# Kernel optimization log

Measured on AMD Instinct MI355X. Metric: run time of the kernel, lower is better.

The kernel has to match this reference:

```python
import jax, jax.numpy as jnp
import numpy as np

DEPTH = 16          # levels in the complete binary tree
D_IN = 256
H = 256
K = 2               # n_children
N_NODES = 2 ** DEPTH - 1  # 65535, heap/level order: children of node p at level l are (2p, 2p+1) at level l+1


def setup_inputs() -> dict:
    key = jax.random.key(0)
    ks = jax.random.split(key, 14)
    s = 0.05
    emb = jax.random.normal(ks[0], (N_NODES, D_IN), dtype=jnp.float32)
    mk = lambda k, shape: (jax.random.normal(k, shape, dtype=jnp.float32) * s)
    return {
        "emb": emb,
        "W_i": mk(ks[1], (H, D_IN)), "b_i": mk(ks[2], (H,)), "U_i": mk(ks[3], (K, H, H)),
        "W_o": mk(ks[4], (H, D_IN)), "b_o": mk(ks[5], (H,)), "U_o": mk(ks[6], (K, H, H)),
        "W_u": mk(ks[7], (H, D_IN)), "b_u": mk(ks[8], (H,)), "U_u": mk(ks[9], (K, H, H)),
        "W_f": mk(ks[10], (H, D_IN)), "b_f": mk(ks[11], (H,)), "U_f": mk(ks[12], (K, H, H)),
    }


def _node_batch(x, ch_h, ch_c, W_i, b_i, U_i, W_o, b_o, U_o, W_u, b_u, U_u, W_f, b_f, U_f):
    # x: [n, D_IN]; ch_h, ch_c: [n, K, H]
    # Linear: x @ W.T + b (torch layout W=[out,in]); U_k h = h @ U[k].T
    def gate(W, b, U):
        return x @ W.T + b + jnp.einsum("nkh,kdh->nd", ch_h, U)
    i = jax.nn.sigmoid(gate(W_i, b_i, U_i))
    o = jax.nn.sigmoid(gate(W_o, b_o, U_o))
    u = jnp.tanh(gate(W_u, b_u, U_u))
    # per-child forget gates: f_k = sigmoid(W_f x + U_f[k] h_k)
    f = jax.nn.sigmoid((x @ W_f.T + b_f)[:, None, :] + jnp.einsum("nkh,kdh->nkd", ch_h, U_f))
    c = i * u + jnp.sum(f * ch_c, axis=1)
    h = o * jnp.tanh(c)
    return h, c


def reference(emb, W_i, b_i, U_i, W_o, b_o, U_o, W_u, b_u, U_u, W_f, b_f, U_f):
    params = (W_i, b_i, U_i, W_o, b_o, U_o, W_u, b_u, U_u, W_f, b_f, U_f)
    # leaves: level DEPTH-1, zero children (matches zero-padding in node_forward)
    n = 2 ** (DEPTH - 1)
    start = n - 1
    zeros = jnp.zeros((n, K, H), dtype=emb.dtype)
    h, c = _node_batch(emb[start:start + n], zeros, zeros, *params)
    # bottom-up over internal levels; children of position p are (2p, 2p+1) in level below
    for l in range(DEPTH - 2, -1, -1):
        n = 2 ** l
        start = n - 1
        ch_h = h.reshape(n, K, H)
        ch_c = c.reshape(n, K, H)
        h, c = _node_batch(emb[start:start + n], ch_h, ch_c, *params)
    return h[0], c[0]  # root (hidden, cell), each [H]
```

## Files before the change

kernel.cpp:

```cpp
#include <hip/hip_runtime.h>
#include <hip/hip_bf16.h>
#include <cstdint>
#include <cstddef>


typedef __attribute__((ext_vector_type(8))) __bf16 bf16x8;
typedef __attribute__((ext_vector_type(4))) float floatx4;

#define TB 64

__device__ __forceinline__ float sigf(float x) { return 1.0f / (1.0f + __expf(-x)); }

__device__ __forceinline__ void load_lds16(const void* g, void* l) {
    __builtin_amdgcn_global_load_lds(
        (const __attribute__((address_space(1))) unsigned int*)g,
        (__attribute__((address_space(3))) unsigned int*)l, 16, 0, 0);
}

__global__ void pack_weights(const float* __restrict__ Wi, const float* __restrict__ bi, const float* __restrict__ Ui,
                             const float* __restrict__ Wo, const float* __restrict__ bo, const float* __restrict__ Uo,
                             const float* __restrict__ Wu, const float* __restrict__ bu, const float* __restrict__ Uu,
                             const float* __restrict__ Wf, const float* __restrict__ bf, const float* __restrict__ Uf,
                             __hip_bfloat16* __restrict__ Wpack, float* __restrict__ biasv)
{
    int m = blockIdx.x;
    int d = blockIdx.y;
    int k = threadIdx.x;
    const float* tbl[12] = {Wi, Wo, Wu, Wf,
                            Ui, Uo, Uu, Uf,
                            Ui + 65536, Uo + 65536, Uu + 65536, Uf + 65536};
    Wpack[((size_t)m * 256 + d) * 256 + k] = __float2bfloat16(tbl[m][d * 256 + k]);
    if (m < 4 && k == 0) {
        const float* bt[4] = {bi, bo, bu, bf};
        biasv[m * 256 + d] = bt[m][d];
    }
}

__global__ void convert_f32_bf16(const float* __restrict__ in, __hip_bfloat16* __restrict__ out, int n4)
{
    int i = blockIdx.x * 256 + threadIdx.x;
    if (i >= n4) return;
    float4 v = ((const float4*)in)[i];
    __hip_bfloat16 tmp[4];
    tmp[0] = __float2bfloat16(v.x);
    tmp[1] = __float2bfloat16(v.y);
    tmp[2] = __float2bfloat16(v.z);
    tmp[3] = __float2bfloat16(v.w);
    *(ushort4*)(out + (size_t)i * 4) = *(const ushort4*)tmp;
}

__global__ __launch_bounds__(256) void gemm_zx(
    const __hip_bfloat16* __restrict__ embB,
    const __hip_bfloat16* __restrict__ Wpack,
    const float* __restrict__ biasv,
    float* __restrict__ preZ,
    int M)
{
    __shared__ __hip_bfloat16 sA[64 * 32];
    __shared__ __hip_bfloat16 sB[64 * 32];
    const int t = threadIdx.x;
    const int s = blockIdx.x >> 2;
    const int d0 = (blockIdx.x & 3) * 64;
    const int bm0 = blockIdx.y * 64;
    const int lane = t & 63, w = t >> 6, lrow = lane & 15, q = lane >> 4;

    floatx4 acc[4];
    #pragma unroll
    for (int mt = 0; mt < 4; ++mt) acc[mt] = (floatx4){0.f, 0.f, 0.f, 0.f};

    for (int kk = 0; kk < 8; ++kk) {
        const int k0 = kk * 32;
        {
            int r = t >> 2, kc = t & 3;
            load_lds16(embB + (size_t)(bm0 + r) * 256 + k0 + kc * 8, &sA[t * 8]);
            load_lds16(Wpack + (size_t)(s * 256 + d0 + r) * 256 + k0 + kc * 8, &sB[t * 8]);
        }
        __syncthreads();
        bf16x8 af[4];
        #pragma unroll
        for (int mt = 0; mt < 4; ++mt)
            af[mt] = *(const bf16x8*)&sA[(mt * 16 + lrow) * 32 + q * 8];
        bf16x8 bfr = *(const bf16x8*)&sB[(w * 16 + lrow) * 32 + q * 8];
        #pragma unroll
        for (int mt = 0; mt < 4; ++mt)
            acc[mt] = __builtin_amdgcn_mfma_f32_16x16x32_bf16(af[mt], bfr, acc[mt], 0, 0, 0);
        __syncthreads();
    }

    const int d = d0 + w * 16 + lrow;
    const float bv = biasv[s * 256 + d];
    #pragma unroll
    for (int mt = 0; mt < 4; ++mt)
        #pragma unroll
        for (int rr = 0; rr < 4; ++rr) {
            int m = bm0 + mt * 16 + q * 4 + rr;
            if (m < M) preZ[(size_t)m * 1024 + s * 256 + d] = acc[mt][rr] + bv;
        }
}

template<int NS, int NP>
__global__ __launch_bounds__(256) void fused_level(
    const __hip_bfloat16* __restrict__ embX,
    const __hip_bfloat16* __restrict__ hprev,
    const float* __restrict__ cprev,
    const __hip_bfloat16* __restrict__ Wpack,
    const float* __restrict__ biasv,
    __hip_bfloat16* __restrict__ hout,
    float* __restrict__ cout,
    int M)
{
    __shared__ __hip_bfloat16 sA[64 * 32];
    __shared__ __hip_bfloat16 sB[NS * 64 * 32];
    const int t = threadIdx.x;
    const int dchunk = blockIdx.x;
    const int bm0 = blockIdx.y * 64;
    const int lane = t & 63;
    const int w = t >> 6;
    const int lrow = lane & 15;
    const int q = lane >> 4;

    floatx4 accS[3][4];
    floatx4 accF[NP][4];
    #pragma unroll
    for (int s = 0; s < 3; ++s)
        #pragma unroll
        for (int mt = 0; mt < 4; ++mt) accS[s][mt] = (floatx4){0.f, 0.f, 0.f, 0.f};
    #pragma unroll
    for (int p = 0; p < NP; ++p)
        #pragma unroll
        for (int mt = 0; mt < 4; ++mt) accF[p][mt] = (floatx4){0.f, 0.f, 0.f, 0.f};

    #pragma unroll
    for (int p = 0; p < NP; ++p) {
        const __hip_bfloat16* Abase = (p == 0) ? embX : hprev;
        const int astride = (p == 0) ? 256 : 512;
        const int aoff = (p == 0) ? 0 : (p - 1) * 256;
        for (int kk = 0; kk < 8; ++kk) {
            const int k0 = kk * 32;
            {
                int r = t >> 2, kc = t & 3;
                load_lds16(Abase + (size_t)(bm0 + r) * astride + aoff + k0 + kc * 8,
                           &sA[t * 8]);
            }
            #pragma unroll
            for (int rep = 0; rep < NS; ++rep) {
                int cid = rep * 256 + t;
                int row = cid >> 2, kc = cid & 3;
                int s = row >> 6, r = row & 63;
                load_lds16(Wpack + (size_t)((p * 4 + s) * 256 + dchunk * 64 + r) * 256 + k0 + kc * 8,
                           &sB[cid * 8]);
            }
            __syncthreads();

            bf16x8 af[4];
            #pragma unroll
            for (int mt = 0; mt < 4; ++mt)
                af[mt] = *(const bf16x8*)&sA[(mt * 16 + lrow) * 32 + q * 8];
            #pragma unroll
            for (int s = 0; s < NS; ++s) {
                bf16x8 bfrag = *(const bf16x8*)&sB[(s * 64 + w * 16 + lrow) * 32 + q * 8];
                if (s < 3) {
                    #pragma unroll
                    for (int mt = 0; mt < 4; ++mt)
                        accS[s][mt] = __builtin_amdgcn_mfma_f32_16x16x32_bf16(af[mt], bfrag, accS[s][mt], 0, 0, 0);
                } else {
                    #pragma unroll
                    for (int mt = 0; mt < 4; ++mt)
                        accF[p][mt] = __builtin_amdgcn_mfma_f32_16x16x32_bf16(af[mt], bfrag, accF[p][mt], 0, 0, 0);
                }
            }
            __syncthreads();
        }
    }

    const int d = dchunk * 64 + w * 16 + lrow;
    const float bI = biasv[d];
    const float bO = biasv[256 + d];
    const float bU = biasv[512 + d];
    const float bF = (NS == 4) ? biasv[768 + d] : 0.0f;
    #pragma unroll
    for (int mt = 0; mt < 4; ++mt) {
        #pragma unroll
        for (int rr = 0; rr < 4; ++rr) {
            const int m = bm0 + mt * 16 + q * 4 + rr;
            if (m >= M) continue;
            float iv = sigf(accS[0][mt][rr] + bI);
            float ov = sigf(accS[1][mt][rr] + bO);
            float uv = tanhf(accS[2][mt][rr] + bU);
            float c;
            if (NS == 4) {
                float fx = accF[0][mt][rr];
                float fl = sigf(fx + accF[NP >= 2 ? 1 : 0][mt][rr] + bF);
                float fr = sigf(fx + accF[NP >= 3 ? 2 : 0][mt][rr] + bF);
                c = iv * uv + fl * cprev[(size_t)m * 512 + d]
                            + fr * cprev[(size_t)m * 512 + 256 + d];
            } else {
                c = iv * uv;
            }
            cout[(size_t)m * 256 + d] = c;
            hout[(size_t)m * 256 + d] = __float2bfloat16(ov * tanhf(c));
        }
    }
}

__global__ __launch_bounds__(256) void tail_levels(
    __hip_bfloat16* __restrict__ hbuf, float* __restrict__ cbuf,
    const __hip_bfloat16* __restrict__ Wpack,
    const float* __restrict__ preZ,
    unsigned* __restrict__ bar, float* __restrict__ out)
{
    __shared__ __hip_bfloat16 sB[8 * 16 * 256];
    const int bid = blockIdx.x;
    const int t = threadIdx.x;
    const int dt = bid & 15;
    const int g = bid >> 4;
    const int w = t >> 6, lane = t & 63, lrow = lane & 15, q = lane >> 4;

    for (int rnd = 0; rnd < 16; ++rnd) {
        int C = rnd * 256 + t;
        int q8k = C & 31, r = (C >> 5) & 15, m8 = C >> 9;
        load_lds16(Wpack + (size_t)((4 + m8) * 256 + dt * 16 + r) * 256 + q8k * 8,
                   &sB[(size_t)C * 8]);
    }
    __syncthreads();

    const int d = dt * 16 + lrow;
    unsigned barnum = 0;

    for (int l = 10; l >= 0; --l) {
        const int n = 1 << l;
        const int start = n - 1;
        const int startc = 2 * n - 1;
        const __hip_bfloat16* hp = hbuf + (size_t)startc * 256;
        const float* cp = cbuf + (size_t)startc * 256;
        __hip_bfloat16* ho = hbuf + (size_t)start * 256;
        float* co = cbuf + (size_t)start * 256;
        const int nmt = (n + 15) >> 4;

        for (int mt = g * 4 + w; mt < nmt; mt += 16) {
            const int m0 = mt * 16;
            bf16x8 af[2][8];
            #pragma unroll
            for (int p = 0; p < 2; ++p)
                #pragma unroll
                for (int kk = 0; kk < 8; ++kk)
                    af[p][kk] = *(const bf16x8*)(hp + (size_t)(m0 + lrow) * 512 + p * 256 + kk * 32 + q * 8);
            float zi[4][4], clr[2][4];
            #pragma unroll
            for (int rr = 0; rr < 4; ++rr) {
                int m = m0 + q * 4 + rr;
                #pragma unroll
                for (int s = 0; s < 4; ++s)
                    zi[s][rr] = preZ[(size_t)(start + m) * 1024 + s * 256 + d];
                clr[0][rr] = cp[(size_t)m * 512 + d];
                clr[1][rr] = cp[(size_t)m * 512 + 256 + d];
            }

            floatx4 accS[3], accF1, accF2;
            #pragma unroll
            for (int s = 0; s < 3; ++s)
                accS[s] = (floatx4){zi[s][0], zi[s][1], zi[s][2], zi[s][3]};
            accF1 = (floatx4){0.f, 0.f, 0.f, 0.f};
            accF2 = (floatx4){0.f, 0.f, 0.f, 0.f};

            #pragma unroll
            for (int p = 0; p < 2; ++p)
                #pragma unroll
                for (int kk = 0; kk < 8; ++kk)
                    #pragma unroll
                    for (int s = 0; s < 4; ++s) {
                        bf16x8 bfr = *(const bf16x8*)&sB[((p * 4 + s) * 16 + lrow) * 256 + kk * 32 + q * 8];
                        if (s < 3)
                            accS[s] = __builtin_amdgcn_mfma_f32_16x16x32_bf16(af[p][kk], bfr, accS[s], 0, 0, 0);
                        else if (p == 0)
                            accF1 = __builtin_amdgcn_mfma_f32_16x16x32_bf16(af[p][kk], bfr, accF1, 0, 0, 0);
                        else
                            accF2 = __builtin_amdgcn_mfma_f32_16x16x32_bf16(af[p][kk], bfr, accF2, 0, 0, 0);
                    }

            #pragma unroll
            for (int rr = 0; rr < 4; ++rr) {
                int m = m0 + q * 4 + rr;
                if (m >= n) continue;
                float iv = sigf(accS[0][rr]);
                float ov = sigf(accS[1][rr]);
                float uv = tanhf(accS[2][rr]);
                float fx = zi[3][rr];
                float fl = sigf(fx + accF1[rr]);
                float fr = sigf(fx + accF2[rr]);
                float c = iv * uv + fl * clr[0][rr] + fr * clr[1][rr];
                float hv = ov * tanhf(c);
                if (l == 0) {
                    out[d] = hv;
                    out[256 + d] = c;
                } else {
                    co[(size_t)m * 256 + d] = c;
                    ho[(size_t)m * 256 + d] = __float2bfloat16(hv);
                }
            }
        }

        if (l > 0) {
            __syncthreads();
            ++barnum;
            if (t == 0) {
                unsigned v = __hip_atomic_fetch_add(&bar[0], 1, __ATOMIC_ACQ_REL,
                                                    __HIP_MEMORY_SCOPE_AGENT) + 1;
                if (v == barnum * (unsigned)TB) {
                    __hip_atomic_fetch_add(&bar[64], 1, __ATOMIC_RELEASE,
                                           __HIP_MEMORY_SCOPE_AGENT);
                } else {
                    while (__hip_atomic_load(&bar[64], __ATOMIC_RELAXED,
                                             __HIP_MEMORY_SCOPE_AGENT) < barnum)
                        __builtin_amdgcn_s_sleep(1);
                }
            }
            __syncthreads();
            __builtin_amdgcn_fence(__ATOMIC_ACQUIRE, "agent");
        }
    }
}

extern "C" void kernel_launch(void* const* d_in, const int* in_sizes, int n_in,
                              void* d_out, int out_size, void* d_ws, size_t ws_size,
                              hipStream_t stream)
{
    const float* emb = (const float*)d_in[0];
    const float* Wi  = (const float*)d_in[1];
    const float* bi  = (const float*)d_in[2];
    const float* Ui  = (const float*)d_in[3];
    const float* Wo  = (const float*)d_in[4];
    const float* bo  = (const float*)d_in[5];
    const float* Uo  = (const float*)d_in[6];
    const float* Wu  = (const float*)d_in[7];
    const float* bu  = (const float*)d_in[8];
    const float* Uu  = (const float*)d_in[9];
    const float* Wf  = (const float*)d_in[10];
    const float* bf  = (const float*)d_in[11];
    const float* Uf  = (const float*)d_in[12];

    char* p = (char*)d_ws;
    __hip_bfloat16* Wpack = (__hip_bfloat16*)p;  p += (size_t)12 * 256 * 256 * 2;
    float* biasv          = (float*)p;           p += (size_t)4 * 256 * 4;
    __hip_bfloat16* embB  = (__hip_bfloat16*)p;  p += (size_t)65535 * 256 * 2;
    __hip_bfloat16* hbuf  = (__hip_bfloat16*)p;  p += (size_t)65535 * 256 * 2;
    float* cbuf           = (float*)p;           p += (size_t)65535 * 256 * 4;
    float* preZ           = (float*)p;           p += (size_t)2047 * 1024 * 4;
    unsigned* bar         = (unsigned*)p;        p += 512;

    pack_weights<<<dim3(12, 256), 256, 0, stream>>>(Wi, bi, Ui, Wo, bo, Uo, Wu, bu, Uu, Wf, bf, Uf,
                                                    Wpack, biasv);
    convert_f32_bf16<<<(65535 * 256 / 4 + 255) / 256, 256, 0, stream>>>(emb, embB, 65535 * 256 / 4);

    gemm_zx<<<dim3(16, 32), 256, 0, stream>>>(embB, Wpack, biasv, preZ, 2047);

    {
        const int n = 32768, start = n - 1;
        fused_level<3, 1><<<dim3(4, n / 64), 256, 0, stream>>>(
            embB + (size_t)start * 256, nullptr, nullptr, Wpack, biasv,
            hbuf + (size_t)start * 256, cbuf + (size_t)start * 256, n);
    }
    for (int l = 14; l >= 11; --l) {
        const int n = 1 << l;
        const int start = n - 1;
        const int startc = 2 * n - 1;
        fused_level<4, 3><<<dim3(4, n / 64), 256, 0, stream>>>(
            embB + (size_t)start * 256,
            hbuf + (size_t)startc * 256,
            cbuf + (size_t)startc * 256,
            Wpack, biasv,
            hbuf + (size_t)start * 256, cbuf + (size_t)start * 256, n);
    }

    hipMemsetAsync(bar, 0, 512, stream);
    tail_levels<<<TB, 256, 0, stream>>>(hbuf, cbuf, Wpack, preZ, bar, (float*)d_out);
}
```

Before: 431.6 us.

## Split tail into grid-barrier levels and single-block final levels with hierarchical barrier

The persistent tail kernel now handles only levels 10..6. It uses a two-level hierarchical grid barrier (group counters of 8 blocks, then a root counter) in place of one flat atomic counter, which cuts contention. Levels 5..0 move to a new single 1024-thread block kernel that uses __syncthreads between levels and reads weights straight from global memory (likely cached). The aim is to remove grid-barrier latency on the tiny upper levels, at the cost of one extra launch and running those levels on a single CU.

```diff
diff --git a/kernel.cpp b/kernel.cpp
--- a/kernel.cpp
+++ b/kernel.cpp
@@ -207,7 +207,7 @@
     __hip_bfloat16* __restrict__ hbuf, float* __restrict__ cbuf,
     const __hip_bfloat16* __restrict__ Wpack,
     const float* __restrict__ preZ,
-    unsigned* __restrict__ bar, float* __restrict__ out)
+    unsigned* __restrict__ bar)
 {
     __shared__ __hip_bfloat16 sB[8 * 16 * 256];
     const int bid = blockIdx.x;
@@ -227,7 +227,112 @@
     const int d = dt * 16 + lrow;
     unsigned barnum = 0;
 
-    for (int l = 10; l >= 0; --l) {
+    for (int l = 10; l >= 6; --l) {
+        const int n = 1 << l;
+        const int start = n - 1;
+        const int startc = 2 * n - 1;
+        const __hip_bfloat16* hp = hbuf + (size_t)startc * 256;
+        const float* cp = cbuf + (size_t)startc * 256;
+        __hip_bfloat16* ho = hbuf + (size_t)start * 256;
+        float* co = cbuf + (size_t)start * 256;
+        const int nmt = n >> 4;
+
+        for (int mt = g * 4 + w; mt < nmt; mt += 16) {
+            const int m0 = mt * 16;
+            bf16x8 af[2][8];
+            #pragma unroll
+            for (int p = 0; p < 2; ++p)
+                #pragma unroll
+                for (int kk = 0; kk < 8; ++kk)
+                    af[p][kk] = *(const bf16x8*)(hp + (size_t)(m0 + lrow) * 512 + p * 256 + kk * 32 + q * 8);
+            float zi[4][4], clr[2][4];
+            #pragma unroll
+            for (int rr = 0; rr < 4; ++rr) {
+                int m = m0 + q * 4 + rr;
+                #pragma unroll
+                for (int s = 0; s < 4; ++s)
+                    zi[s][rr] = preZ[(size_t)(start + m) * 1024 + s * 256 + d];
+                clr[0][rr] = cp[(size_t)m * 512 + d];
+                clr[1][rr] = cp[(size_t)m * 512 + 256 + d];
+            }
+
+            floatx4 accS[3], accF1, accF2;
+            #pragma unroll
+            for (int s = 0; s < 3; ++s)
+                accS[s] = (floatx4){zi[s][0], zi[s][1], zi[s][2], zi[s][3]};
+            accF1 = (floatx4){0.f, 0.f, 0.f, 0.f};
+            accF2 = (floatx4){0.f, 0.f, 0.f, 0.f};
+
+            #pragma unroll
+            for (int p = 0; p < 2; ++p)
+                #pragma unroll
+                for (int kk = 0; kk < 8; ++kk)
+                    #pragma unroll
+                    for (int s = 0; s < 4; ++s) {
+                        bf16x8 bfr = *(const bf16x8*)&sB[((p * 4 + s) * 16 + lrow) * 256 + kk * 32 + q * 8];
+                        if (s < 3)
+                            accS[s] = __builtin_amdgcn_mfma_f32_16x16x32_bf16(af[p][kk], bfr, accS[s], 0, 0, 0);
+                        else if (p == 0)
+                            accF1 = __builtin_amdgcn_mfma_f32_16x16x32_bf16(af[p][kk], bfr, accF1, 0, 0, 0);
+                        else
+                            accF2 = __builtin_amdgcn_mfma_f32_16x16x32_bf16(af[p][kk], bfr, accF2, 0, 0, 0);
+                    }
+
+            #pragma unroll
+            for (int rr = 0; rr < 4; ++rr) {
+                int m = m0 + q * 4 + rr;
+                float iv = sigf(accS[0][rr]);
+                float ov = sigf(accS[1][rr]);
+                float uv = tanhf(accS[2][rr]);
+                float fx = zi[3][rr];
+                float fl = sigf(fx + accF1[rr]);
+                float fr = sigf(fx + accF2[rr]);
+                float c = iv * uv + fl * clr[0][rr] + fr * clr[1][rr];
+                co[(size_t)m * 256 + d] = c;
+                ho[(size_t)m * 256 + d] = __float2bfloat16(ov * tanhf(c));
+            }
+        }
+
+        if (l > 6) {
+            __syncthreads();
+            ++barnum;
+            if (t == 0) {
+                unsigned* gcnt = &bar[(bid >> 3) * 32];
+                bool done = false;
+                unsigned v = __hip_atomic_fetch_add(gcnt, 1, __ATOMIC_RELEASE,
+                                                    __HIP_MEMORY_SCOPE_AGENT) + 1;
+                if (v == barnum * 8u) {
+                    unsigned r = __hip_atomic_fetch_add(&bar[256], 1, __ATOMIC_RELEASE,
+                                                        __HIP_MEMORY_SCOPE_AGENT) + 1;
+                    if (r == barnum * 8u) {
+                        __hip_atomic_store(&bar[288], barnum, __ATOMIC_RELEASE,
+                                           __HIP_MEMORY_SCOPE_AGENT);
+                        done = true;
+                    }
+                }
+                if (!done)
+                    while (__hip_atomic_load(&bar[288], __ATOMIC_RELAXED,
+                                             __HIP_MEMORY_SCOPE_AGENT) < barnum)
+                        __builtin_amdgcn_s_sleep(1);
+            }
+            __syncthreads();
+            __builtin_amdgcn_fence(__ATOMIC_ACQUIRE, "agent");
+        }
+    }
+}
+
+__global__ __launch_bounds__(1024) void final_levels(
+    __hip_bfloat16* __restrict__ hbuf, float* __restrict__ cbuf,
+    const __hip_bfloat16* __restrict__ Wpack,
+    const float* __restrict__ preZ,
+    float* __restrict__ out)
+{
+    const int t = threadIdx.x;
+    const int wave = t >> 6;
+    const int lane = t & 63, lrow = lane & 15, q = lane >> 4;
+    const int d = wave * 16 + lrow;
+
+    for (int l = 5; l >= 0; --l) {
         const int n = 1 << l;
         const int start = n - 1;
         const int startc = 2 * n - 1;
@@ -237,7 +342,7 @@
         float* co = cbuf + (size_t)start * 256;
         const int nmt = (n + 15) >> 4;
 
-        for (int mt = g * 4 + w; mt < nmt; mt += 16) {
+        for (int mt = 0; mt < nmt; ++mt) {
             const int m0 = mt * 16;
             bf16x8 af[2][8];
             #pragma unroll
@@ -269,7 +374,8 @@
                 for (int kk = 0; kk < 8; ++kk)
                     #pragma unroll
                     for (int s = 0; s < 4; ++s) {
-                        bf16x8 bfr = *(const bf16x8*)&sB[((p * 4 + s) * 16 + lrow) * 256 + kk * 32 + q * 8];
+                        bf16x8 bfr = *(const bf16x8*)(Wpack +
+                            (size_t)((4 + p * 4 + s) * 256 + wave * 16 + lrow) * 256 + kk * 32 + q * 8);
                         if (s < 3)
                             accS[s] = __builtin_amdgcn_mfma_f32_16x16x32_bf16(af[p][kk], bfr, accS[s], 0, 0, 0);
                         else if (p == 0)
@@ -299,25 +405,7 @@
                 }
             }
         }
-
-        if (l > 0) {
-            __syncthreads();
-            ++barnum;
-            if (t == 0) {
-                unsigned v = __hip_atomic_fetch_add(&bar[0], 1, __ATOMIC_ACQ_REL,
-                                                    __HIP_MEMORY_SCOPE_AGENT) + 1;
-                if (v == barnum * (unsigned)TB) {
-                    __hip_atomic_fetch_add(&bar[64], 1, __ATOMIC_RELEASE,
-                                           __HIP_MEMORY_SCOPE_AGENT);
-                } else {
-                    while (__hip_atomic_load(&bar[64], __ATOMIC_RELAXED,
-                                             __HIP_MEMORY_SCOPE_AGENT) < barnum)
-                        __builtin_amdgcn_s_sleep(1);
-                }
-            }
-            __syncthreads();
-            __builtin_amdgcn_fence(__ATOMIC_ACQUIRE, "agent");
-        }
+        __syncthreads();
     }
 }
 
@@ -346,7 +434,7 @@
     __hip_bfloat16* hbuf  = (__hip_bfloat16*)p;  p += (size_t)65535 * 256 * 2;
     float* cbuf           = (float*)p;           p += (size_t)65535 * 256 * 4;
     float* preZ           = (float*)p;           p += (size_t)2047 * 1024 * 4;
-    unsigned* bar         = (unsigned*)p;        p += 512;
+    unsigned* bar         = (unsigned*)p;        p += 2048;
 
     pack_weights<<<dim3(12, 256), 256, 0, stream>>>(Wi, bi, Ui, Wo, bo, Uo, Wu, bu, Uu, Wf, bf, Uf,
                                                     Wpack, biasv);
@@ -372,6 +460,7 @@
             hbuf + (size_t)start * 256, cbuf + (size_t)start * 256, n);
     }
 
-    hipMemsetAsync(bar, 0, 512, stream);
-    tail_levels<<<TB, 256, 0, stream>>>(hbuf, cbuf, Wpack, preZ, bar, (float*)d_out);
-}
+    hipMemsetAsync(bar, 0, 2048, stream);
+    tail_levels<<<TB, 256, 0, stream>>>(hbuf, cbuf, Wpack, preZ, bar);
+    final_levels<<<1, 1024, 0, stream>>>(hbuf, cbuf, Wpack, preZ, (float*)d_out);
+}
```

Result: slower. 931.0 us (+115.7%).

## Use weight-stationary level kernels with LDS-resident U tiles and hierarchical grid barrier

Applied to the files above, without the earlier changes.

The per-level GEMM kernels are replaced by a weight-stationary design. Each block loads the U weights for a 16-column d-slice into LDS once, using a rotated swizzle to avoid bank conflicts, then loops over row tiles. A-fragments are read directly from global memory and W_x fragments come from global/L2, which removes the per-k-step LDS staging and syncthreads. The tail kernel's grid barrier becomes two-level, with group counters before a global counter, to cut atomic contention, and the root output write is guarded. The cost is larger LDS use (one block per CU) and uncached global A reads.

```diff
diff --git a/kernel.cpp b/kernel.cpp
--- a/kernel.cpp
+++ b/kernel.cpp
@@ -98,8 +98,8 @@
         }
 }
 
-template<int NS, int NP>
-__global__ __launch_bounds__(256) void fused_level(
+template<bool LEAF>
+__global__ __launch_bounds__(256, 1) void wstat_level(
     const __hip_bfloat16* __restrict__ embX,
     const __hip_bfloat16* __restrict__ hprev,
     const float* __restrict__ cprev,
@@ -107,98 +107,102 @@
     const float* __restrict__ biasv,
     __hip_bfloat16* __restrict__ hout,
     float* __restrict__ cout,
-    int M)
-{
-    __shared__ __hip_bfloat16 sA[64 * 32];
-    __shared__ __hip_bfloat16 sB[NS * 64 * 32];
+    int n, int G)
+{
+    constexpr int NMAT = LEAF ? 3 : 8;
+    __shared__ __hip_bfloat16 sU[NMAT * 16 * 256];
     const int t = threadIdx.x;
-    const int dchunk = blockIdx.x;
-    const int bm0 = blockIdx.y * 64;
-    const int lane = t & 63;
-    const int w = t >> 6;
-    const int lrow = lane & 15;
-    const int q = lane >> 4;
-
-    floatx4 accS[3][4];
-    floatx4 accF[NP][4];
+    const int dt = blockIdx.x & 15;
+    const int g  = blockIdx.x >> 4;
+    const int w = t >> 6, lane = t & 63, lrow = lane & 15, q = lane >> 4;
+
     #pragma unroll
-    for (int s = 0; s < 3; ++s)
-        #pragma unroll
-        for (int mt = 0; mt < 4; ++mt) accS[s][mt] = (floatx4){0.f, 0.f, 0.f, 0.f};
-    #pragma unroll
-    for (int p = 0; p < NP; ++p)
-        #pragma unroll
-        for (int mt = 0; mt < 4; ++mt) accF[p][mt] = (floatx4){0.f, 0.f, 0.f, 0.f};
-
-    #pragma unroll
-    for (int p = 0; p < NP; ++p) {
-        const __hip_bfloat16* Abase = (p == 0) ? embX : hprev;
-        const int astride = (p == 0) ? 256 : 512;
-        const int aoff = (p == 0) ? 0 : (p - 1) * 256;
-        for (int kk = 0; kk < 8; ++kk) {
-            const int k0 = kk * 32;
-            {
-                int r = t >> 2, kc = t & 3;
-                load_lds16(Abase + (size_t)(bm0 + r) * astride + aoff + k0 + kc * 8,
-                           &sA[t * 8]);
-            }
-            #pragma unroll
-            for (int rep = 0; rep < NS; ++rep) {
-                int cid = rep * 256 + t;
-                int row = cid >> 2, kc = cid & 3;
-                int s = row >> 6, r = row & 63;
-                load_lds16(Wpack + (size_t)((p * 4 + s) * 256 + dchunk * 64 + r) * 256 + k0 + kc * 8,
-                           &sB[cid * 8]);
-            }
-            __syncthreads();
-
-            bf16x8 af[4];
-            #pragma unroll
-            for (int mt = 0; mt < 4; ++mt)
-                af[mt] = *(const bf16x8*)&sA[(mt * 16 + lrow) * 32 + q * 8];
-            #pragma unroll
-            for (int s = 0; s < NS; ++s) {
-                bf16x8 bfrag = *(const bf16x8*)&sB[(s * 64 + w * 16 + lrow) * 32 + q * 8];
-                if (s < 3) {
-                    #pragma unroll
-                    for (int mt = 0; mt < 4; ++mt)
-                        accS[s][mt] = __builtin_amdgcn_mfma_f32_16x16x32_bf16(af[mt], bfrag, accS[s][mt], 0, 0, 0);
+    for (int it = 0; it < NMAT * 2; ++it) {
+        int cid = it * 256 + t;
+        int mat = cid >> 9;
+        int row = (cid >> 5) & 15;
+        int sl  = cid & 31;
+        int cc  = (sl - 4 * (row & 7)) & 31;
+        load_lds16(Wpack + (size_t)(((LEAF ? 0 : 4) + mat) * 256 + dt * 16 + row) * 256 + cc * 8,
+                   &sU[cid * 8]);
+    }
+    __syncthreads();
+
+    const int rot = q + 4 * (lrow & 7);
+    const int d = dt * 16 + lrow;
+    const float bI = biasv[d], bO = biasv[256 + d], bU = biasv[512 + d];
+    const float bF = LEAF ? 0.0f : biasv[768 + d];
+
+    const int stmax = n >> 6;
+    for (int st = g * 4 + w; st < stmax; st += G * 4) {
+        const int m0 = st * 64;
+        floatx4 accS[3][4];
+        floatx4 accF[3][4];
+        #pragma unroll
+        for (int s = 0; s < 3; ++s)
+            #pragma unroll
+            for (int mt = 0; mt < 4; ++mt) {
+                accS[s][mt] = (floatx4){0.f, 0.f, 0.f, 0.f};
+                accF[s][mt] = (floatx4){0.f, 0.f, 0.f, 0.f};
+            }
+
+        #pragma unroll
+        for (int p = 0; p < (LEAF ? 1 : 3); ++p) {
+            const __hip_bfloat16* Ab = (p == 0) ? embX : hprev;
+            const int astr = (p == 0) ? 256 : 512;
+            const int aoff = (p == 0) ? 0 : (p - 1) * 256;
+            #pragma unroll
+            for (int kk = 0; kk < 8; ++kk) {
+                bf16x8 af[4];
+                #pragma unroll
+                for (int mt = 0; mt < 4; ++mt)
+                    af[mt] = *(const bf16x8*)(Ab + (size_t)(m0 + mt * 16 + lrow) * astr + aoff + kk * 32 + q * 8);
+                #pragma unroll
+                for (int s = 0; s < (LEAF ? 3 : 4); ++s) {
+                    bf16x8 bfr;
+                    if (LEAF) {
+                        int sl = (kk * 4 + rot) & 31;
+                        bfr = *(const bf16x8*)&sU[(s * 16 + lrow) * 256 + sl * 8];
+                    } else if (p == 0) {
+                        bfr = *(const bf16x8*)(Wpack + (size_t)(s * 256 + dt * 16 + lrow) * 256 + kk * 32 + q * 8);
+                    } else {
+                        int sl = (kk * 4 + rot) & 31;
+                        bfr = *(const bf16x8*)&sU[(((p - 1) * 4 + s) * 16 + lrow) * 256 + sl * 8];
+                    }
+                    if (s < 3) {
+                        #pragma unroll
+                        for (int mt = 0; mt < 4; ++mt)
+                            accS[s][mt] = __builtin_amdgcn_mfma_f32_16x16x32_bf16(af[mt], bfr, accS[s][mt], 0, 0, 0);
+                    } else {
+                        #pragma unroll
+                        for (int mt = 0; mt < 4; ++mt)
+                            accF[p][mt] = __builtin_amdgcn_mfma_f32_16x16x32_bf16(af[mt], bfr, accF[p][mt], 0, 0, 0);
+                    }
+                }
+            }
+        }
+
+        #pragma unroll
+        for (int mt = 0; mt < 4; ++mt) {
+            #pragma unroll
+            for (int rr = 0; rr < 4; ++rr) {
+                const int m = m0 + mt * 16 + q * 4 + rr;
+                float iv = sigf(accS[0][mt][rr] + bI);
+                float ov = sigf(accS[1][mt][rr] + bO);
+                float uv = tanhf(accS[2][mt][rr] + bU);
+                float c;
+                if (LEAF) {
+                    c = iv * uv;
                 } else {
-                    #pragma unroll
-                    for (int mt = 0; mt < 4; ++mt)
-                        accF[p][mt] = __builtin_amdgcn_mfma_f32_16x16x32_bf16(af[mt], bfrag, accF[p][mt], 0, 0, 0);
+                    float fx = accF[0][mt][rr];
+                    float fl = sigf(fx + accF[1][mt][rr] + bF);
+                    float fr = sigf(fx + accF[2][mt][rr] + bF);
+                    c = iv * uv + fl * cprev[(size_t)m * 512 + d]
+                                + fr * cprev[(size_t)m * 512 + 256 + d];
                 }
-            }
-            __syncthreads();
-        }
-    }
-
-    const int d = dchunk * 64 + w * 16 + lrow;
-    const float bI = biasv[d];
-    const float bO = biasv[256 + d];
-    const float bU = biasv[512 + d];
-    const float bF = (NS == 4) ? biasv[768 + d] : 0.0f;
-    #pragma unroll
-    for (int mt = 0; mt < 4; ++mt) {
-        #pragma unroll
-        for (int rr = 0; rr < 4; ++rr) {
-            const int m = bm0 + mt * 16 + q * 4 + rr;
-            if (m >= M) continue;
-            float iv = sigf(accS[0][mt][rr] + bI);
-            float ov = sigf(accS[1][mt][rr] + bO);
-            float uv = tanhf(accS[2][mt][rr] + bU);
-            float c;
-            if (NS == 4) {
-                float fx = accF[0][mt][rr];
-                float fl = sigf(fx + accF[NP >= 2 ? 1 : 0][mt][rr] + bF);
-                float fr = sigf(fx + accF[NP >= 3 ? 2 : 0][mt][rr] + bF);
-                c = iv * uv + fl * cprev[(size_t)m * 512 + d]
-                            + fr * cprev[(size_t)m * 512 + 256 + d];
-            } else {
-                c = iv * uv;
-            }
-            cout[(size_t)m * 256 + d] = c;
-            hout[(size_t)m * 256 + d] = __float2bfloat16(ov * tanhf(c));
+                cout[(size_t)m * 256 + d] = c;
+                hout[(size_t)m * 256 + d] = __float2bfloat16(ov * tanhf(c));
+            }
         }
     }
 }
@@ -291,8 +295,7 @@
                 float c = iv * uv + fl * clr[0][rr] + fr * clr[1][rr];
                 float hv = ov * tanhf(c);
                 if (l == 0) {
-                    out[d] = hv;
-                    out[256 + d] = c;
+                    if (m == 0) { out[d] = hv; out[256 + d] = c; }
                 } else {
                     co[(size_t)m * 256 + d] = c;
                     ho[(size_t)m * 256 + d] = __float2bfloat16(hv);
@@ -304,16 +307,23 @@
             __syncthreads();
             ++barnum;
             if (t == 0) {
-                unsigned v = __hip_atomic_fetch_add(&bar[0], 1, __ATOMIC_ACQ_REL,
+                unsigned* gcnt = &bar[(bid >> 3) * 32];
+                bool done = false;
+                unsigned v = __hip_atomic_fetch_add(gcnt, 1, __ATOMIC_RELEASE,
                                                     __HIP_MEMORY_SCOPE_AGENT) + 1;
-                if (v == barnum * (unsigned)TB) {
-                    __hip_atomic_fetch_add(&bar[64], 1, __ATOMIC_RELEASE,
+                if (v == barnum * 8u) {
+                    unsigned r = __hip_atomic_fetch_add(&bar[256], 1, __ATOMIC_RELEASE,
+                                                        __HIP_MEMORY_SCOPE_AGENT) + 1;
+                    if (r == barnum * 8u) {
+                        __hip_atomic_store(&bar[288], barnum, __ATOMIC_RELEASE,
                                            __HIP_MEMORY_SCOPE_AGENT);
-                } else {
-                    while (__hip_atomic_load(&bar[64], __ATOMIC_RELAXED,
+                        done = true;
+                    }
+                }
+                if (!done)
+                    while (__hip_atomic_load(&bar[288], __ATOMIC_RELAXED,
                                              __HIP_MEMORY_SCOPE_AGENT) < barnum)
                         __builtin_amdgcn_s_sleep(1);
-                }
             }
             __syncthreads();
             __builtin_amdgcn_fence(__ATOMIC_ACQUIRE, "agent");
@@ -346,7 +356,7 @@
     __hip_bfloat16* hbuf  = (__hip_bfloat16*)p;  p += (size_t)65535 * 256 * 2;
     float* cbuf           = (float*)p;           p += (size_t)65535 * 256 * 4;
     float* preZ           = (float*)p;           p += (size_t)2047 * 1024 * 4;
-    unsigned* bar         = (unsigned*)p;        p += 512;
+    unsigned* bar         = (unsigned*)p;        p += 2048;
 
     pack_weights<<<dim3(12, 256), 256, 0, stream>>>(Wi, bi, Ui, Wo, bo, Uo, Wu, bu, Uu, Wf, bf, Uf,
                                                     Wpack, biasv);
@@ -356,22 +366,22 @@
 
     {
         const int n = 32768, start = n - 1;
-        fused_level<3, 1><<<dim3(4, n / 64), 256, 0, stream>>>(
+        wstat_level<true><<<16 * 64, 256, 0, stream>>>(
             embB + (size_t)start * 256, nullptr, nullptr, Wpack, biasv,
-            hbuf + (size_t)start * 256, cbuf + (size_t)start * 256, n);
+            hbuf + (size_t)start * 256, cbuf + (size_t)start * 256, n, 64);
     }
     for (int l = 14; l >= 11; --l) {
         const int n = 1 << l;
         const int start = n - 1;
         const int startc = 2 * n - 1;
-        fused_level<4, 3><<<dim3(4, n / 64), 256, 0, stream>>>(
+        wstat_level<false><<<16 * 32, 256, 0, stream>>>(
             embB + (size_t)start * 256,
             hbuf + (size_t)startc * 256,
             cbuf + (size_t)startc * 256,
             Wpack, biasv,
-            hbuf + (size_t)start * 256, cbuf + (size_t)start * 256, n);
-    }
-
-    hipMemsetAsync(bar, 0, 512, stream);
+            hbuf + (size_t)start * 256, cbuf + (size_t)start * 256, n, 32);
+    }
+
+    hipMemsetAsync(bar, 0, 2048, stream);
     tail_levels<<<TB, 256, 0, stream>>>(hbuf, cbuf, Wpack, preZ, bar, (float*)d_out);
 }
```

Measured after the change: 605.3 us. 40.3% more time.

## Use hierarchical grid barrier and agent-scope atomic accesses for inter-level data

Applied to the files above, without the earlier changes.

The persistent tail kernel's grid barrier becomes two-level: blocks arrive on one of eight group counters, and the last arriver of each group increments a root counter whose final arriver publishes a release flag. Shared h/c data between levels is now read and written with relaxed agent-scope atomic loads and stores, so the post-barrier acquire fence can be narrowed from agent to workgroup scope, avoiding cache invalidation. The aim is to cut barrier contention and fence cost across the 11 tail levels. It relies on subtle memory-ordering reasoning, and the per-element atomic loads and stores may be slower than plain vector accesses.

```diff
diff --git a/kernel.cpp b/kernel.cpp
--- a/kernel.cpp
+++ b/kernel.cpp
@@ -15,6 +15,26 @@
     __builtin_amdgcn_global_load_lds(
         (const __attribute__((address_space(1))) unsigned int*)g,
         (__attribute__((address_space(3))) unsigned int*)l, 16, 0, 0);
+}
+
+__device__ __forceinline__ bf16x8 load_h16_llc(const __hip_bfloat16* p) {
+    const unsigned long long* q = (const unsigned long long*)p;
+    union { unsigned long long u[2]; bf16x8 v; } u;
+    u.u[0] = __hip_atomic_load(&q[0], __ATOMIC_RELAXED, __HIP_MEMORY_SCOPE_AGENT);
+    u.u[1] = __hip_atomic_load(&q[1], __ATOMIC_RELAXED, __HIP_MEMORY_SCOPE_AGENT);
+    return u.v;
+}
+__device__ __forceinline__ float load_f_llc(const float* p) {
+    return __hip_atomic_load(p, __ATOMIC_RELAXED, __HIP_MEMORY_SCOPE_AGENT);
+}
+__device__ __forceinline__ void store_f_llc(float* p, float v) {
+    __hip_atomic_store(p, v, __ATOMIC_RELAXED, __HIP_MEMORY_SCOPE_AGENT);
+}
+__device__ __forceinline__ void store_h_llc(__hip_bfloat16* p, float v) {
+    __hip_bfloat16 h = __float2bfloat16(v);
+    unsigned short u;
+    __builtin_memcpy(&u, &h, 2);
+    __hip_atomic_store((unsigned short*)p, u, __ATOMIC_RELAXED, __HIP_MEMORY_SCOPE_AGENT);
 }
 
 __global__ void pack_weights(const float* __restrict__ Wi, const float* __restrict__ bi, const float* __restrict__ Ui,
@@ -244,7 +264,7 @@
             for (int p = 0; p < 2; ++p)
                 #pragma unroll
                 for (int kk = 0; kk < 8; ++kk)
-                    af[p][kk] = *(const bf16x8*)(hp + (size_t)(m0 + lrow) * 512 + p * 256 + kk * 32 + q * 8);
+                    af[p][kk] = load_h16_llc(hp + (size_t)(m0 + lrow) * 512 + p * 256 + kk * 32 + q * 8);
             float zi[4][4], clr[2][4];
             #pragma unroll
             for (int rr = 0; rr < 4; ++rr) {
@@ -252,8 +272,8 @@
                 #pragma unroll
                 for (int s = 0; s < 4; ++s)
                     zi[s][rr] = preZ[(size_t)(start + m) * 1024 + s * 256 + d];
-                clr[0][rr] = cp[(size_t)m * 512 + d];
-                clr[1][rr] = cp[(size_t)m * 512 + 256 + d];
+                clr[0][rr] = load_f_llc(cp + (size_t)m * 512 + d);
+                clr[1][rr] = load_f_llc(cp + (size_t)m * 512 + 256 + d);
             }
 
             floatx4 accS[3], accF1, accF2;
@@ -291,11 +311,10 @@
                 float c = iv * uv + fl * clr[0][rr] + fr * clr[1][rr];
                 float hv = ov * tanhf(c);
                 if (l == 0) {
-                    out[d] = hv;
-                    out[256 + d] = c;
+                    if (m == 0) { out[d] = hv; out[256 + d] = c; }
                 } else {
-                    co[(size_t)m * 256 + d] = c;
-                    ho[(size_t)m * 256 + d] = __float2bfloat16(hv);
+                    store_f_llc(co + (size_t)m * 256 + d, c);
+                    store_h_llc(ho + (size_t)m * 256 + d, hv);
                 }
             }
         }
@@ -304,19 +323,26 @@
             __syncthreads();
             ++barnum;
             if (t == 0) {
-                unsigned v = __hip_atomic_fetch_add(&bar[0], 1, __ATOMIC_ACQ_REL,
+                unsigned* gcnt = &bar[(bid >> 3) * 32];
+                bool done = false;
+                unsigned v = __hip_atomic_fetch_add(gcnt, 1, __ATOMIC_RELEASE,
                                                     __HIP_MEMORY_SCOPE_AGENT) + 1;
-                if (v == barnum * (unsigned)TB) {
-                    __hip_atomic_fetch_add(&bar[64], 1, __ATOMIC_RELEASE,
+                if (v == barnum * 8u) {
+                    unsigned r = __hip_atomic_fetch_add(&bar[256], 1, __ATOMIC_RELEASE,
+                                                        __HIP_MEMORY_SCOPE_AGENT) + 1;
+                    if (r == barnum * 8u) {
+                        __hip_atomic_store(&bar[288], barnum, __ATOMIC_RELEASE,
                                            __HIP_MEMORY_SCOPE_AGENT);
-                } else {
-                    while (__hip_atomic_load(&bar[64], __ATOMIC_RELAXED,
+                        done = true;
+                    }
+                }
+                if (!done)
+                    while (__hip_atomic_load(&bar[288], __ATOMIC_RELAXED,
                                              __HIP_MEMORY_SCOPE_AGENT) < barnum)
                         __builtin_amdgcn_s_sleep(1);
-                }
             }
             __syncthreads();
-            __builtin_amdgcn_fence(__ATOMIC_ACQUIRE, "agent");
+            __builtin_amdgcn_fence(__ATOMIC_ACQUIRE, "workgroup");
         }
     }
 }
@@ -346,7 +372,7 @@
     __hip_bfloat16* hbuf  = (__hip_bfloat16*)p;  p += (size_t)65535 * 256 * 2;
     float* cbuf           = (float*)p;           p += (size_t)65535 * 256 * 4;
     float* preZ           = (float*)p;           p += (size_t)2047 * 1024 * 4;
-    unsigned* bar         = (unsigned*)p;        p += 512;
+    unsigned* bar         = (unsigned*)p;        p += 2048;
 
     pack_weights<<<dim3(12, 256), 256, 0, stream>>>(Wi, bi, Ui, Wo, bo, Uo, Wu, bu, Uu, Wf, bf, Uf,
                                                     Wpack, biasv);
@@ -372,6 +398,6 @@
             hbuf + (size_t)start * 256, cbuf + (size_t)start * 256, n);
     }
 
-    hipMemsetAsync(bar, 0, 512, stream);
+    hipMemsetAsync(bar, 0, 2048, stream);
     tail_levels<<<TB, 256, 0, stream>>>(hbuf, cbuf, Wpack, preZ, bar, (float*)d_out);
 }
```

Result: slower. 443.2 us (+2.7%).
